# Optimization experiments

Measured on AMD Instinct MI355X. Metric: run time of the kernel, lower is better.

The kernel has to match this reference:

```python
import jax, jax.numpy as jnp
import numpy as np

EMBED_DIM = 1024
FFN_DIM = 4096
N_QUBITS = 10


def setup_inputs() -> dict:
    key = jax.random.key(0)
    k_x, k_phi, k_w1, k_w2 = jax.random.split(key, 4)
    x = jax.random.normal(k_x, (8, 2048, EMBED_DIM), dtype=jnp.float32)
    # trainable RY angles, one per wire (torchquantum init ~ U(0, 2pi); any init works for a reference)
    ry_params = jax.random.uniform(k_phi, (N_QUBITS,), dtype=jnp.float32, minval=0.0, maxval=2.0 * np.pi)
    # nn.Linear(n_qubits, ffn_dim, bias=False): weight [ffn_dim, n_qubits]
    w1 = jax.random.normal(k_w1, (FFN_DIM, N_QUBITS), dtype=jnp.float32) / np.sqrt(N_QUBITS)
    # nn.Linear(ffn_dim, embed_dim, bias=False): weight [embed_dim, ffn_dim]
    w2 = jax.random.normal(k_w2, (EMBED_DIM, FFN_DIM), dtype=jnp.float32) / np.sqrt(FFN_DIM)
    return {"x": x, "ry_params": ry_params, "w1": w1, "w2": w2}


def reference(x, ry_params, w1, w2):
    # Quantum layer in closed form: wires are unentangled.
    # |0> --RX(x_i)--RY(phi_i)--> <Z_i> = cos(x_i) * cos(phi_i)
    # Only the first N_QUBITS features of each token are encoded.
    q_out = jnp.cos(x[..., :N_QUBITS]) * jnp.cos(ry_params)  # [B, S, nq]
    # dropout is identity in eval mode
    h = jnp.einsum('bsq,fq->bsf', q_out, w1)  # [B, S, ffn]
    h = jax.nn.relu(h)
    return jnp.einsum('bsf,ef->bse', h, w2)  # [B, S, embed]
```

## Files before the change

### kernel.cpp

```cpp
#include <hip/hip_runtime.h>
#include <stdint.h>

#define M_TOK   16384
#define EMBED   1024
#define FFN     4096
#define NQ      10

#define GK 4096
#define GN 1024
#define BK 64
#define NT (GK / BK)

typedef __attribute__((ext_vector_type(8))) short  bf16x8;
typedef __attribute__((ext_vector_type(4))) float  f32x4;
typedef __attribute__((ext_vector_type(8))) unsigned short u16x8;

static __device__ __forceinline__ unsigned short f2bf(float f) {
    union { float f; unsigned u; } v; v.f = f;
    unsigned r = v.u + 0x7FFF + ((v.u >> 16) & 1);
    return (unsigned short)(r >> 16);
}

__global__ __launch_bounds__(256) void prep_w1(
    const float* __restrict__ w1, const float* __restrict__ ry,
    float* __restrict__ w1cT)
{
    __shared__ float cry[16];
    if (threadIdx.x < NQ) cry[threadIdx.x] = cosf(ry[threadIdx.x]);
    __syncthreads();
    const int f = blockIdx.x * 256 + threadIdx.x;
#pragma unroll
    for (int i = 0; i < NQ; ++i)
        w1cT[i * FFN + f] = w1[f * NQ + i] * cry[i];
}

__global__ __launch_bounds__(256) void compute_h(
    const float* __restrict__ x, const float* __restrict__ w1cT,
    unsigned short* __restrict__ h)
{
    __shared__ float cq[32 * 16];

    const int tid = threadIdx.x;
    const int t0  = blockIdx.x * 32;
    const int fb  = blockIdx.y * 2048 + tid * 8;

    for (int idx = tid; idx < 32 * NQ; idx += 256) {
        int t = idx / NQ;
        int i = idx - t * NQ;
        cq[t * 16 + i] = cosf(x[(size_t)(t0 + t) * EMBED + i]);
    }
    __syncthreads();

    float wf[8][NQ];
#pragma unroll
    for (int i = 0; i < NQ; ++i) {
        const float4 lo = *(const float4*)(w1cT + (size_t)i * FFN + fb);
        const float4 hi = *(const float4*)(w1cT + (size_t)i * FFN + fb + 4);
        wf[0][i] = lo.x; wf[1][i] = lo.y; wf[2][i] = lo.z; wf[3][i] = lo.w;
        wf[4][i] = hi.x; wf[5][i] = hi.y; wf[6][i] = hi.z; wf[7][i] = hi.w;
    }

    for (int t = 0; t < 32; ++t) {
        const float4 c0 = *(const float4*)&cq[t * 16 + 0];
        const float4 c1 = *(const float4*)&cq[t * 16 + 4];
        const float2 c2 = *(const float2*)&cq[t * 16 + 8];
        u16x8 v;
#pragma unroll
        for (int fi = 0; fi < 8; ++fi) {
            float s = c0.x * wf[fi][0] + c0.y * wf[fi][1] + c0.z * wf[fi][2]
                    + c0.w * wf[fi][3] + c1.x * wf[fi][4] + c1.y * wf[fi][5]
                    + c1.z * wf[fi][6] + c1.w * wf[fi][7] + c2.x * wf[fi][8]
                    + c2.y * wf[fi][9];
            v[fi] = f2bf(fmaxf(s, 0.f));
        }
        *(u16x8*)(h + (size_t)(t0 + t) * FFN + fb) = v;
    }
}

__global__ __launch_bounds__(256) void conv_w2(
    const float* __restrict__ w2, unsigned short* __restrict__ o)
{
    const int idx = (blockIdx.x * 256 + threadIdx.x) * 8;
    float4 a = *(const float4*)(w2 + idx);
    float4 b = *(const float4*)(w2 + idx + 4);
    u16x8 v;
    v[0] = f2bf(a.x); v[1] = f2bf(a.y); v[2] = f2bf(a.z); v[3] = f2bf(a.w);
    v[4] = f2bf(b.x); v[5] = f2bf(b.y); v[6] = f2bf(b.z); v[7] = f2bf(b.w);
    *(u16x8*)(o + idx) = v;
}

#define GL2LDS(g, l) \
    __builtin_amdgcn_global_load_lds( \
        (const __attribute__((address_space(1))) void*)(g), \
        (__attribute__((address_space(3))) void*)(l), 16, 0, 0)

__global__ __launch_bounds__(512, 2) void gemm_bt(
    const unsigned short* __restrict__ A,
    const unsigned short* __restrict__ B,
    float* __restrict__ C)
{
    __shared__ __align__(16) unsigned short As[2][256 * BK];
    __shared__ __align__(16) unsigned short Bs[2][256 * BK];

    const int tid  = threadIdx.x;
    const int wv   = tid >> 6;
    const int lane = tid & 63;
    const int wm   = wv >> 2;
    const int wn   = wv & 3;

    const int bid = blockIdx.x;
    const int wg  = (bid & 7) * 32 + (bid >> 3);
    const int m0  = (wg >> 2) * 256;
    const int n0  = (wg & 3) * 256;

    const int srow8 = lane >> 3;
    const int schk  = (lane & 7) ^ srow8;
    const char* ag = (const char*)A +
        ((size_t)(m0 + wv * 16 + srow8) * GK + schk * 8) * 2;
    const char* bg = (const char*)B +
        ((size_t)(n0 + wv * 16 + srow8) * GK + schk * 8) * 2;
    const size_t ROW8 = (size_t)8 * GK * 2;
    const size_t HALF = (size_t)128 * GK * 2;

#define STAGE_A(buf, half, ko) do { \
    GL2LDS(ag + (ko) + (half) * HALF,        (char*)As[buf] + ((half) * 128 + wv * 16) * 128); \
    GL2LDS(ag + (ko) + (half) * HALF + ROW8, (char*)As[buf] + ((half) * 128 + wv * 16 + 8) * 128); \
} while (0)
#define STAGE_B(buf, half, ko) do { \
    GL2LDS(bg + (ko) + (half) * HALF,        (char*)Bs[buf] + ((half) * 128 + wv * 16) * 128); \
    GL2LDS(bg + (ko) + (half) * HALF + ROW8, (char*)Bs[buf] + ((half) * 128 + wv * 16 + 8) * 128); \
} while (0)
#define STAGE_ALL(buf, ko) do { \
    STAGE_A(buf, 0, ko); STAGE_A(buf, 1, ko); \
    STAGE_B(buf, 0, ko); STAGE_B(buf, 1, ko); \
} while (0)

    const int rr  = lane & 15;
    const int fsw = lane & 7;
    const int cc  = lane >> 4;
#define CHOFF(s) ((((s) * 4 + cc) ^ fsw) * 16)
#define RD_A(dst, Pt, mh) do { \
    _Pragma("unroll") \
    for (int s_ = 0; s_ < 2; ++s_) \
        _Pragma("unroll") \
        for (int i_ = 0; i_ < 4; ++i_) \
            dst[s_][i_] = *(const bf16x8*)((Pt) + \
                (wm * 128 + (mh) * 64 + i_ * 16 + rr) * 128 + CHOFF(s_)); \
} while (0)
#define RD_B(dst, Pt, nh) do { \
    _Pragma("unroll") \
    for (int s_ = 0; s_ < 2; ++s_) \
        _Pragma("unroll") \
        for (int j_ = 0; j_ < 2; ++j_) \
            dst[s_][j_] = *(const bf16x8*)((Pt) + \
                (wn * 64 + (nh) * 32 + j_ * 16 + rr) * 128 + CHOFF(s_)); \
} while (0)

    f32x4 acc[8][4] = {};

#define MFMA16(AF, BF, I0, J0) do { \
    __builtin_amdgcn_s_setprio(1); \
    _Pragma("unroll") \
    for (int s_ = 0; s_ < 2; ++s_) \
        _Pragma("unroll") \
        for (int i_ = 0; i_ < 4; ++i_) \
            _Pragma("unroll") \
            for (int j_ = 0; j_ < 2; ++j_) \
                acc[(I0) + i_][(J0) + j_] = __builtin_amdgcn_mfma_f32_16x16x32_bf16( \
                    AF[s_][i_], BF[s_][j_], acc[(I0) + i_][(J0) + j_], 0, 0, 0); \
    __builtin_amdgcn_s_setprio(0); \
} while (0)

    bf16x8 aA[2][4], aB[2][4], bP[2][2], bQ[2][2];

    STAGE_ALL(0, 0);
    STAGE_ALL(1, 128);
    asm volatile("s_waitcnt vmcnt(8)" ::: "memory");
    __builtin_amdgcn_s_barrier();
    RD_A(aA, (const char*)As[0], 0);
    RD_B(bP, (const char*)Bs[0], 0);

#define TILE(T, cur, nxt, BPm, BQm, doRead, doStage, ko2) do { \
    const char* At = (const char*)As[cur]; \
    const char* Bt = (const char*)Bs[cur]; \
     \
    RD_B(BQm, Bt, 1); \
    MFMA16(aA, BPm, 0, 0); \
     \
    RD_A(aB, At, 1); \
    MFMA16(aA, BQm, 0, 2); \
     \
    MFMA16(aB, BQm, 4, 2); \
    asm volatile("s_waitcnt vmcnt(0)" ::: "memory"); \
    __builtin_amdgcn_s_barrier(); \
    __builtin_amdgcn_sched_barrier(0); \
     \
    if (doRead) { \
        const char* An = (const char*)As[nxt]; \
        const char* Bn = (const char*)Bs[nxt]; \
        RD_A(aA, An, 0); \
        RD_B(BQm, Bn, 0); \
    } \
    if (doStage) STAGE_ALL(cur, ko2); \
    MFMA16(aB, BPm, 4, 0); \
} while (0)

#pragma unroll 1
    for (int tt = 0; tt < NT / 2; ++tt) {
        const bool nl = (tt < NT / 2 - 1);
        TILE(2 * tt, 0, 1, bP, bQ, true, nl, (size_t)(2 * tt + 2) * 128);
        TILE(2 * tt + 1, 1, 0, bQ, bP, nl, nl, (size_t)(2 * tt + 3) * 128);
    }

    const int cn = lane & 15;
    const int rb = (lane >> 4) * 4;
#pragma unroll
    for (int i = 0; i < 8; ++i)
#pragma unroll
        for (int j = 0; j < 4; ++j)
#pragma unroll
            for (int r = 0; r < 4; ++r) {
                const int m = m0 + wm * 128 + i * 16 + rb + r;
                const int n = n0 + wn * 64 + j * 16 + cn;
                C[(size_t)m * GN + n] = acc[i][j][r];
            }
}

extern "C" void kernel_launch(void* const* d_in, const int* in_sizes, int n_in,
                              void* d_out, int out_size, void* d_ws, size_t ws_size,
                              hipStream_t stream) {
    const float* x  = (const float*)d_in[0];
    const float* ry = (const float*)d_in[1];
    const float* w1 = (const float*)d_in[2];
    const float* w2 = (const float*)d_in[3];
    float* out = (float*)d_out;

    unsigned short* h   = (unsigned short*)d_ws;
    unsigned short* w2b = (unsigned short*)((char*)d_ws +
                           (size_t)M_TOK * FFN * sizeof(unsigned short));
    float* w1cT = (float*)w2b;

    prep_w1<<<dim3(FFN / 256), 256, 0, stream>>>(w1, ry, w1cT);
    compute_h<<<dim3(512, 2), 256, 0, stream>>>(x, w1cT, h);
    conv_w2<<<dim3((EMBED * FFN) / (256 * 8)), 256, 0, stream>>>(w2, w2b);
    gemm_bt<<<dim3(256), 512, 0, stream>>>(h, w2b, out);
}
```

Before: 255.5 us.

## Restructure GEMM main loop into 4-phase ping-pong schedule with interleaved staging

Rewrites the bf16 GEMM inner loop so each K tile is processed in four MFMA phases, each bracketed by barriers and preceded by one quarter of the next tile's global-to-LDS staging. Wave-to-tile mapping changes so each wave's fragments are split across the two 128-row/col halves, which changes the LDS read addresses and the output indexing. The aim is finer-grained overlap of global loads, LDS reads and MFMA across the two co-resident workgroups, and fewer live fragment registers. The cost is many more barriers per tile, and a single fragment buffer means LDS reads can no longer be issued ahead of the preceding MFMAs.

```diff
diff --git a/kernel.cpp b/kernel.cpp
--- a/kernel.cpp
+++ b/kernel.cpp
@@ -129,10 +129,6 @@
 #define STAGE_B(buf, half, ko) do { \
     GL2LDS(bg + (ko) + (half) * HALF,        (char*)Bs[buf] + ((half) * 128 + wv * 16) * 128); \
     GL2LDS(bg + (ko) + (half) * HALF + ROW8, (char*)Bs[buf] + ((half) * 128 + wv * 16 + 8) * 128); \
-} while (0)
-#define STAGE_ALL(buf, ko) do { \
-    STAGE_A(buf, 0, ko); STAGE_A(buf, 1, ko); \
-    STAGE_B(buf, 0, ko); STAGE_B(buf, 1, ko); \
 } while (0)
 
     const int rr  = lane & 15;
@@ -145,7 +141,7 @@
         _Pragma("unroll") \
         for (int i_ = 0; i_ < 4; ++i_) \
             dst[s_][i_] = *(const bf16x8*)((Pt) + \
-                (wm * 128 + (mh) * 64 + i_ * 16 + rr) * 128 + CHOFF(s_)); \
+                ((mh) * 128 + wm * 64 + i_ * 16 + rr) * 128 + CHOFF(s_)); \
 } while (0)
 #define RD_B(dst, Pt, nh) do { \
     _Pragma("unroll") \
@@ -153,7 +149,7 @@
         _Pragma("unroll") \
         for (int j_ = 0; j_ < 2; ++j_) \
             dst[s_][j_] = *(const bf16x8*)((Pt) + \
-                (wn * 64 + (nh) * 32 + j_ * 16 + rr) * 128 + CHOFF(s_)); \
+                ((nh) * 128 + wn * 32 + j_ * 16 + rr) * 128 + CHOFF(s_)); \
 } while (0)
 
     f32x4 acc[8][4] = {};
@@ -171,46 +167,54 @@
     __builtin_amdgcn_s_setprio(0); \
 } while (0)
 
-    bf16x8 aA[2][4], aB[2][4], bP[2][2], bQ[2][2];
-
-    STAGE_ALL(0, 0);
-    STAGE_ALL(1, 128);
-    asm volatile("s_waitcnt vmcnt(8)" ::: "memory");
+#define SYNC_IN do { \
+    __builtin_amdgcn_s_barrier(); \
+    asm volatile("s_waitcnt lgkmcnt(0)" ::: "memory"); \
+    __builtin_amdgcn_sched_barrier(0); \
+} while (0)
+#define SYNC_OUT do { \
+    asm volatile("s_waitcnt vmcnt(4)" ::: "memory"); \
+    __builtin_amdgcn_s_barrier(); \
+} while (0)
+
+    bf16x8 aF[2][4], b0[2][2], b1[2][2];
+
+    STAGE_A(0, 0, 0); STAGE_B(0, 0, 0);
+    STAGE_B(0, 1, 0); STAGE_A(0, 1, 0);
+    asm volatile("s_waitcnt vmcnt(4)" ::: "memory");
     __builtin_amdgcn_s_barrier();
-    RD_A(aA, (const char*)As[0], 0);
-    RD_B(bP, (const char*)Bs[0], 0);
-
-#define TILE(T, cur, nxt, BPm, BQm, doRead, doStage, ko2) do { \
+
+#define TILE4(cur, SH1, SH2, SH3, SH4) do { \
     const char* At = (const char*)As[cur]; \
     const char* Bt = (const char*)Bs[cur]; \
      \
-    RD_B(BQm, Bt, 1); \
-    MFMA16(aA, BPm, 0, 0); \
-     \
-    RD_A(aB, At, 1); \
-    MFMA16(aA, BQm, 0, 2); \
-     \
-    MFMA16(aB, BQm, 4, 2); \
-    asm volatile("s_waitcnt vmcnt(0)" ::: "memory"); \
-    __builtin_amdgcn_s_barrier(); \
-    __builtin_amdgcn_sched_barrier(0); \
-     \
-    if (doRead) { \
-        const char* An = (const char*)As[nxt]; \
-        const char* Bn = (const char*)Bs[nxt]; \
-        RD_A(aA, An, 0); \
-        RD_B(BQm, Bn, 0); \
-    } \
-    if (doStage) STAGE_ALL(cur, ko2); \
-    MFMA16(aB, BPm, 4, 0); \
+    RD_A(aF, At, 0); RD_B(b0, Bt, 0); \
+    SH1; \
+    SYNC_IN; MFMA16(aF, b0, 0, 0); SYNC_OUT; \
+     \
+    RD_B(b1, Bt, 1); \
+    SH2; \
+    SYNC_IN; MFMA16(aF, b1, 0, 2); SYNC_OUT; \
+     \
+    RD_A(aF, At, 1); \
+    SH3; \
+    SYNC_IN; MFMA16(aF, b1, 4, 2); SYNC_OUT; \
+     \
+    SH4; \
+    SYNC_IN; MFMA16(aF, b0, 4, 0); SYNC_OUT; \
 } while (0)
 
 #pragma unroll 1
     for (int tt = 0; tt < NT / 2; ++tt) {
-        const bool nl = (tt < NT / 2 - 1);
-        TILE(2 * tt, 0, 1, bP, bQ, true, nl, (size_t)(2 * tt + 2) * 128);
-        TILE(2 * tt + 1, 1, 0, bQ, bP, nl, nl, (size_t)(2 * tt + 3) * 128);
-    }
+        const size_t kv = (size_t)(2 * tt + 1) * 128;
+        const size_t ku = (2 * tt + 2 < NT) ? (size_t)(2 * tt + 2) * 128 : 0;
+        TILE4(0, STAGE_A(1, 0, kv), STAGE_B(1, 0, kv),
+                 STAGE_B(1, 1, kv), STAGE_A(1, 1, kv));
+        TILE4(1, STAGE_A(0, 0, ku), STAGE_B(0, 0, ku),
+                 STAGE_B(0, 1, ku), STAGE_A(0, 1, ku));
+    }
+
+    asm volatile("s_waitcnt vmcnt(0)" ::: "memory");
 
     const int cn = lane & 15;
     const int rb = (lane >> 4) * 4;
@@ -220,8 +224,8 @@
         for (int j = 0; j < 4; ++j)
 #pragma unroll
             for (int r = 0; r < 4; ++r) {
-                const int m = m0 + wm * 128 + i * 16 + rb + r;
-                const int n = n0 + wn * 64 + j * 16 + cn;
+                const int m = m0 + (i >> 2) * 128 + wm * 64 + (i & 3) * 16 + rb + r;
+                const int n = n0 + (j >> 1) * 128 + wn * 32 + (j & 1) * 16 + cn;
                 C[(size_t)m * GN + n] = acc[i][j][r];
             }
 }
```

Result: slower. 280.8 us (+9.9%).
